# Performance work log

Hardware: AMD Instinct MI355X
Metric: run time of the kernel (lower is better)

The kernel has to match this reference:

```python
import jax, jax.numpy as jnp
import numpy as np

B, T, C, H = 4, 4096, 1024, 64

def setup_inputs() -> dict:
    key = jax.random.key(0)
    k1, k2, k3, k4 = jax.random.split(key, 4)
    x = jax.random.normal(k1, (B, T, C), dtype=jnp.float32)
    # nn.Linear(C, H, bias=False): y = x @ W^T with W [H, C]; store as [C, H] for x @ W
    Wq = jax.random.normal(k2, (C, H), dtype=jnp.float32) * (C ** -0.5)
    Wk = jax.random.normal(k3, (C, H), dtype=jnp.float32) * (C ** -0.5)
    Wv = jax.random.normal(k4, (C, H), dtype=jnp.float32) * (C ** -0.5)
    return {"x": x, "Wq": Wq, "Wk": Wk, "Wv": Wv}

def reference(x, Wq, Wk, Wv):
    # Manual causal single-head attention (dropout p=0 -> identity).
    q = x @ Wq  # [B, T, H]
    k = x @ Wk  # [B, T, H]
    v = x @ Wv  # [B, T, H]
    scale = q.shape[-1] ** -0.5
    w = jnp.einsum('bth,bsh->bts', q, k) * scale  # [B, T, T] scores
    causal = jnp.tril(jnp.ones((x.shape[1], x.shape[1]), dtype=bool))
    w = jnp.where(causal, w, -jnp.inf)
    w = jax.nn.softmax(w, axis=-1)
    out = jnp.einsum('bts,bsh->bth', w, v)  # [B, T, H]
    return out
```

## Files before the change

### kernel.cpp

```cpp
#include <hip/hip_runtime.h>
#include <math.h>

#define Bn 4
#define Tn 4096
#define Cn 1024
#define Hn 64

typedef __attribute__((ext_vector_type(8))) short short8;
typedef __attribute__((ext_vector_type(4))) float floatx4;
typedef unsigned short ushort_t;

#define QSCALE 0.1803368801111204f

#define ILP_FENCE() asm volatile("" ::: "memory")

__device__ __forceinline__ ushort_t f2bf(float f) {
  union { float f; unsigned u; } v; v.f = f;
  unsigned r = v.u + 0x7FFFu + ((v.u >> 16) & 1u);
  return (ushort_t)(r >> 16);
}
__device__ __forceinline__ ushort_t f2bf_hu(float f) {
  union { float f; unsigned u; } v; v.f = f;
  return (ushort_t)((v.u + 0x8000u) >> 16);
}
__device__ __forceinline__ float bf2f(ushort_t h) {
  union { unsigned u; float f; } v; v.u = ((unsigned)h) << 16; return v.f;
}


__global__ __launch_bounds__(256) void wf_kernel(
    const float* __restrict__ Wq, const float* __restrict__ Wk,
    const float* __restrict__ Wv, ushort_t* __restrict__ Wf)
{
  __shared__ float ws[32][65];
  const int tid = threadIdx.x;
  const int m = blockIdx.x >> 5;
  const int g = blockIdx.x & 31;
  const float* W = (m == 0) ? Wq : (m == 1) ? Wk : Wv;
  const float4* src = (const float4*)(W + (size_t)g * 32 * Hn);
#pragma unroll
  for (int it = 0; it < 2; ++it) {
    int i4 = it * 256 + tid;
    float4 v = src[i4];
    int c = i4 >> 4, h = (i4 & 15) * 4;
    ws[c][h] = v.x; ws[c][h + 1] = v.y; ws[c][h + 2] = v.z; ws[c][h + 3] = v.w;
  }
  __syncthreads();
  const int nt = tid >> 6, lane = tid & 63;
  const int col = lane & 15, quad = lane >> 4;
  ushort_t t[8];
#pragma unroll
  for (int e = 0; e < 8; ++e) t[e] = f2bf(ws[quad * 8 + e][nt * 16 + col]);
  *(short8*)(Wf + ((size_t)((m * 32 + g) * 4 + nt) * 64 + lane) * 8) = *(short8*)t;
}

__global__ __launch_bounds__(256, 2) void qkv_proj_kernel(
    const float* __restrict__ x, const ushort_t* __restrict__ Wf,
    ushort_t* __restrict__ Qf, ushort_t* __restrict__ Kf,
    ushort_t* __restrict__ Vf)
{
  __shared__ __align__(16) char smem[67584];
  ushort_t* xs  = (ushort_t*)smem;
  ushort_t* red = (ushort_t*)smem;
  ushort_t* img = (ushort_t*)(smem + 49152);

  const int tid  = threadIdx.x;
  const int wv   = tid >> 6;
  const int lane = tid & 63;
  const int col  = lane & 15;
  const int quad = lane >> 4;
  const int blk  = blockIdx.x;
  const int row0 = blk * 32;

#pragma unroll
  for (int half = 0; half < 2; ++half) {
    float4 v[16];
#pragma unroll
    for (int jj = 0; jj < 16; ++jj)
      v[jj] = *(const float4*)(x + (size_t)(row0 + half * 16 + jj) * Cn + wv * 256 + lane * 4);
    ILP_FENCE();
#pragma unroll
    for (int jj = 0; jj < 16; ++jj) {
      ushort4 u;
      u.x = f2bf(v[jj].x); u.y = f2bf(v[jj].y); u.z = f2bf(v[jj].z); u.w = f2bf(v[jj].w);
      *(ushort4*)(xs + (wv * 32 + half * 16 + jj) * 264 + lane * 4) = u;
    }
  }

  floatx4 acc[2][3][4];
#pragma unroll
  for (int sub = 0; sub < 2; ++sub)
#pragma unroll
    for (int m = 0; m < 3; ++m)
#pragma unroll
      for (int nt = 0; nt < 4; ++nt) {
        acc[sub][m][nt][0] = 0.f; acc[sub][m][nt][1] = 0.f;
        acc[sub][m][nt][2] = 0.f; acc[sub][m][nt][3] = 0.f;
      }

#pragma unroll
  for (int ch = 0; ch < 8; ++ch) {
    const int gg = wv * 8 + ch;
    short8 bf[12];
#pragma unroll
    for (int k = 0; k < 12; ++k) {
      const int m_ = k >> 2, nt_ = k & 3;
      bf[k] = *(const short8*)(Wf + ((size_t)((m_ * 32 + gg) * 4 + nt_) * 64 + lane) * 8);
    }
    short8 af0 = *(const short8*)(xs + (wv * 32 + col) * 264 + ch * 32 + quad * 8);
    short8 af1 = *(const short8*)(xs + (wv * 32 + 16 + col) * 264 + ch * 32 + quad * 8);
    ILP_FENCE();
#pragma unroll
    for (int k = 0; k < 12; ++k) {
      const int m_ = k >> 2, nt_ = k & 3;
      acc[0][m_][nt_] = __builtin_amdgcn_mfma_f32_16x16x32_bf16(af0, bf[k], acc[0][m_][nt_], 0, 0, 0);
      acc[1][m_][nt_] = __builtin_amdgcn_mfma_f32_16x16x32_bf16(af1, bf[k], acc[1][m_][nt_], 0, 0, 0);
    }
  }
  __syncthreads();

#pragma unroll
  for (int sub = 0; sub < 2; ++sub)
#pragma unroll
    for (int m = 0; m < 3; ++m)
#pragma unroll
      for (int nt = 0; nt < 4; ++nt) {
        const int p = (sub * 3 + m) * 4 + nt;
        ushort4 u;
        u.x = f2bf(acc[sub][m][nt][0]); u.y = f2bf(acc[sub][m][nt][1]);
        u.z = f2bf(acc[sub][m][nt][2]); u.w = f2bf(acc[sub][m][nt][3]);
        *(ushort4*)&red[((p * 4 + wv) * 64 + lane) * 4] = u;
      }
  __syncthreads();

#pragma unroll
  for (int pp = 0; pp < 6; ++pp) {
    const int p = wv * 6 + pp;
    ushort4 w0 = *(const ushort4*)&red[((p * 4 + 0) * 64 + lane) * 4];
    ushort4 w1 = *(const ushort4*)&red[((p * 4 + 1) * 64 + lane) * 4];
    ushort4 w2 = *(const ushort4*)&red[((p * 4 + 2) * 64 + lane) * 4];
    ushort4 w3 = *(const ushort4*)&red[((p * 4 + 3) * 64 + lane) * 4];
    float v[4];
    v[0] = (bf2f(w0.x) + bf2f(w1.x)) + (bf2f(w2.x) + bf2f(w3.x));
    v[1] = (bf2f(w0.y) + bf2f(w1.y)) + (bf2f(w2.y) + bf2f(w3.y));
    v[2] = (bf2f(w0.z) + bf2f(w1.z)) + (bf2f(w2.z) + bf2f(w3.z));
    v[3] = (bf2f(w0.w) + bf2f(w1.w)) + (bf2f(w2.w) + bf2f(w3.w));
    const int sub = (p >= 12) ? 1 : 0;
    const int mrem = p - sub * 12;
    const int m = mrem >> 2, nt = mrem & 3;
#pragma unroll
    for (int r = 0; r < 4; ++r) {
      const int tlq = quad * 4 + r;
      if (m == 2) {
        img[4096 + nt * 512 + (quad * 16 + col) * 8 + sub * 4 + r] = f2bf(v[r]);
      } else {
        const int h = nt * 16 + col;
        const int idx = (h >> 5) * 512 + ((h >> 3) & 3) * 128 + tlq * 8 + (h & 7);
        img[m * 2048 + sub * 1024 + idx] = f2bf(m == 0 ? v[r] * QSCALE : v[r]);
      }
    }
  }
  __syncthreads();

  {
    const int b = blk >> 7, g = blk & 127;
#pragma unroll
    for (int sub = 0; sub < 2; ++sub) {
      const size_t qg = (size_t)(b * 256 + 2 * g + sub) * 1024 + tid * 4;
      *(uint2*)(Qf + qg) = *(const uint2*)&img[sub * 1024 + tid * 4];
      *(uint2*)(Kf + qg) = *(const uint2*)&img[2048 + sub * 1024 + tid * 4];
    }
    const int ht = tid >> 6;
    const size_t vg = ((size_t)(b * 64 + (g >> 1)) * 8 + ht * 2 + (g & 1)) * 512 + (tid & 63) * 8;
    *(short8*)(Vf + vg) = *(const short8*)&img[4096 + ht * 512 + (tid & 63) * 8];
  }
}

__global__ __launch_bounds__(256, 2) void attn_kernel(
    const ushort_t* __restrict__ Qf, const ushort_t* __restrict__ Kf,
    const ushort_t* __restrict__ Vf, float* __restrict__ out)
{
  __shared__ __align__(16) float Om[4][2][16][68];
  __shared__ __align__(16) float Ml[4][2][16];

  const int tid  = threadIdx.x;
  const int wv   = tid >> 6;
  const int lane = tid & 63;
  const int col  = lane & 15;
  const int quad = lane >> 4;
  const int b   = blockIdx.x & 3;
  const int idx = blockIdx.x >> 2;
  const int g   = (idx < 64) ? (127 - 2 * idx) : (2 * (idx - 64));

  short8 qf[2][2];
#pragma unroll
  for (int sub = 0; sub < 2; ++sub)
#pragma unroll
    for (int half = 0; half < 2; ++half)
      qf[sub][half] = *(const short8*)(Qf + (size_t)(b * 256 + 2 * g + sub) * 1024 + half * 512 + lane * 8);

  const ushort_t* Kbase = Kf + (size_t)b * 256 * 1024;
  const ushort_t* Vbase = Vf + (size_t)b * 64 * 8 * 512;

  short8 ones;
#pragma unroll
  for (int e = 0; e < 8; ++e) ones[e] = (short)0x3F80;

  floatx4 o[2][4], ol[2];
#pragma unroll
  for (int sub = 0; sub < 2; ++sub) {
#pragma unroll
    for (int ht = 0; ht < 4; ++ht) { o[sub][ht][0]=0.f; o[sub][ht][1]=0.f; o[sub][ht][2]=0.f; o[sub][ht][3]=0.f; }
    ol[sub][0]=0.f; ol[sub][1]=0.f; ol[sub][2]=0.f; ol[sub][3]=0.f;
  }

  const int ntile = ((g * 32 + 31) >> 6) + 1;
  const int dtile = ntile - 1;

  for (int i = wv; i < ntile; i += 4) {
    short8 kf[8], vf[8];
#pragma unroll
    for (int kt = 0; kt < 4; ++kt) {
      const ushort_t* kp = Kbase + (size_t)i * 4096 + kt * 1024 + lane * 8;
      kf[kt * 2]     = *(const short8*)(kp);
      kf[kt * 2 + 1] = *(const short8*)(kp + 512);
    }
#pragma unroll
    for (int ht = 0; ht < 4; ++ht) {
#pragma unroll
      for (int kh = 0; kh < 2; ++kh)
        vf[ht * 2 + kh] = *(const short8*)(Vbase + ((size_t)i * 8 + ht * 2 + kh) * 512 + lane * 8);
    }
    ILP_FENCE();

    floatx4 s[2][4];
    __builtin_amdgcn_s_setprio(1);
#pragma unroll
    for (int sub = 0; sub < 2; ++sub)
#pragma unroll
      for (int kt = 0; kt < 4; ++kt) {
        floatx4 c; c[0]=0.f; c[1]=0.f; c[2]=0.f; c[3]=0.f;
        c = __builtin_amdgcn_mfma_f32_16x16x32_bf16(kf[kt * 2],     qf[sub][0], c, 0, 0, 0);
        c = __builtin_amdgcn_mfma_f32_16x16x32_bf16(kf[kt * 2 + 1], qf[sub][1], c, 0, 0, 0);
        s[sub][kt] = c;
      }
    __builtin_amdgcn_s_setprio(0);

    if (i == dtile) {
#pragma unroll
      for (int sub = 0; sub < 2; ++sub)
#pragma unroll
        for (int kt = 0; kt < 4; ++kt)
#pragma unroll
          for (int r = 0; r < 4; ++r)
            if (64 * i + kt * 16 + quad * 4 + r > g * 32 + sub * 16 + col)
              s[sub][kt][r] = -INFINITY;
    }

#pragma unroll
    for (int sub = 0; sub < 2; ++sub)
#pragma unroll
      for (int kt = 0; kt < 4; ++kt)
#pragma unroll
        for (int r = 0; r < 4; ++r)
          s[sub][kt][r] = __builtin_amdgcn_exp2f(s[sub][kt][r]);

    short8 pf[2][2];
#pragma unroll
    for (int sub = 0; sub < 2; ++sub)
#pragma unroll
      for (int kh = 0; kh < 2; ++kh) {
        ushort_t tmp[8];
#pragma unroll
        for (int half = 0; half < 2; ++half)
#pragma unroll
          for (int r = 0; r < 4; ++r)
            tmp[half * 4 + r] = f2bf_hu(s[sub][2 * kh + half][r]);
        pf[sub][kh] = *(short8*)tmp;
      }

    __builtin_amdgcn_s_setprio(1);
#pragma unroll
    for (int sub = 0; sub < 2; ++sub) {
#pragma unroll
      for (int ht = 0; ht < 4; ++ht) {
        o[sub][ht] = __builtin_amdgcn_mfma_f32_16x16x32_bf16(pf[sub][0], vf[ht * 2],     o[sub][ht], 0, 0, 0);
        o[sub][ht] = __builtin_amdgcn_mfma_f32_16x16x32_bf16(pf[sub][1], vf[ht * 2 + 1], o[sub][ht], 0, 0, 0);
      }
      ol[sub] = __builtin_amdgcn_mfma_f32_16x16x32_bf16(pf[sub][0], ones, ol[sub], 0, 0, 0);
      ol[sub] = __builtin_amdgcn_mfma_f32_16x16x32_bf16(pf[sub][1], ones, ol[sub], 0, 0, 0);
    }
    __builtin_amdgcn_s_setprio(0);
  }

#pragma unroll
  for (int sub = 0; sub < 2; ++sub) {
#pragma unroll
    for (int ht = 0; ht < 4; ++ht)
#pragma unroll
      for (int r = 0; r < 4; ++r)
        Om[wv][sub][quad * 4 + r][ht * 16 + col] = o[sub][ht][r];
    if (col == 0) {
#pragma unroll
      for (int r = 0; r < 4; ++r) Ml[wv][sub][quad * 4 + r] = ol[sub][r];
    }
  }
  __syncthreads();

  const int rr = tid >> 4, h4 = (tid & 15) * 4;
#pragma unroll
  for (int sub = 0; sub < 2; ++sub) {
    float L = (Ml[0][sub][rr] + Ml[1][sub][rr]) + (Ml[2][sub][rr] + Ml[3][sub][rr]);
    float4 a; a.x = 0.f; a.y = 0.f; a.z = 0.f; a.w = 0.f;
#pragma unroll
    for (int w = 0; w < 4; ++w) {
      float4 ov = *(const float4*)&Om[w][sub][rr][h4];
      a.x += ov.x; a.y += ov.y; a.z += ov.z; a.w += ov.w;
    }
    float inv = 1.f / L;
    a.x *= inv; a.y *= inv; a.z *= inv; a.w *= inv;
    *(float4*)(out + (size_t)(b * Tn + g * 32 + sub * 16 + rr) * Hn + h4) = a;
  }
}

extern "C" void kernel_launch(void* const* d_in, const int* in_sizes, int n_in,
                              void* d_out, int out_size, void* d_ws, size_t ws_size,
                              hipStream_t stream) {
  const float* x  = (const float*)d_in[0];
  const float* Wq = (const float*)d_in[1];
  const float* Wk = (const float*)d_in[2];
  const float* Wv = (const float*)d_in[3];
  float* out = (float*)d_out;

  ushort_t* Qf = (ushort_t*)d_ws;
  ushort_t* Kf = Qf + (size_t)Bn * Tn * Hn;
  ushort_t* Vf = Kf + (size_t)Bn * Tn * Hn;
  ushort_t* Wf = Vf + (size_t)Bn * Tn * Hn;

  wf_kernel<<<dim3(96), dim3(256), 0, stream>>>(Wq, Wk, Wv, Wf);
  qkv_proj_kernel<<<dim3(512), dim3(256), 0, stream>>>(x, Wf, Qf, Kf, Vf);
  attn_kernel<<<dim3(Bn * 128), dim3(256), 0, stream>>>(Qf, Kf, Vf, out);
}
```

Baseline: 123.3 us.

## Load x via direct global-to-LDS DMA and halve projection block rows

The QKV projection kernel now stages fp32 x rows straight into shared memory with global_load_lds, using an XOR swizzle, instead of loading into registers, converting to bf16 and storing. Conversion to bf16 moves to the A-fragment read inside the MFMA loop. Each block now handles 16 rows rather than 32, so twice as many blocks are launched and each keeps half as many accumulators, with the Q/K/V write-out indexing updated to match. The aim is to reduce register pressure and staging overhead and to raise parallelism, at the cost of reloading the weight fragments from global memory in twice as many blocks.

```diff
diff --git a/kernel.cpp b/kernel.cpp
--- a/kernel.cpp
+++ b/kernel.cpp
@@ -13,6 +13,12 @@
 #define QSCALE 0.1803368801111204f
 
 #define ILP_FENCE() asm volatile("" ::: "memory")
+
+__device__ __forceinline__ void dma16(const void* g, void* l) {
+  __builtin_amdgcn_global_load_lds(
+      (const __attribute__((address_space(1))) void*)g,
+      (__attribute__((address_space(3))) void*)l, 16, 0, 0);
+}
 
 __device__ __forceinline__ ushort_t f2bf(float f) {
   union { float f; unsigned u; } v; v.f = f;
@@ -59,10 +65,9 @@
     ushort_t* __restrict__ Qf, ushort_t* __restrict__ Kf,
     ushort_t* __restrict__ Vf)
 {
-  __shared__ __align__(16) char smem[67584];
-  ushort_t* xs  = (ushort_t*)smem;
+  __shared__ __align__(16) char smem[65536];
   ushort_t* red = (ushort_t*)smem;
-  ushort_t* img = (ushort_t*)(smem + 49152);
+  ushort_t* img = (ushort_t*)(smem + 24576);
 
   const int tid  = threadIdx.x;
   const int wv   = tid >> 6;
@@ -70,33 +75,25 @@
   const int col  = lane & 15;
   const int quad = lane >> 4;
   const int blk  = blockIdx.x;
-  const int row0 = blk * 32;
-
-#pragma unroll
-  for (int half = 0; half < 2; ++half) {
-    float4 v[16];
-#pragma unroll
-    for (int jj = 0; jj < 16; ++jj)
-      v[jj] = *(const float4*)(x + (size_t)(row0 + half * 16 + jj) * Cn + wv * 256 + lane * 4);
-    ILP_FENCE();
-#pragma unroll
-    for (int jj = 0; jj < 16; ++jj) {
-      ushort4 u;
-      u.x = f2bf(v[jj].x); u.y = f2bf(v[jj].y); u.z = f2bf(v[jj].z); u.w = f2bf(v[jj].w);
-      *(ushort4*)(xs + (wv * 32 + half * 16 + jj) * 264 + lane * 4) = u;
-    }
-  }
-
-  floatx4 acc[2][3][4];
-#pragma unroll
-  for (int sub = 0; sub < 2; ++sub)
-#pragma unroll
-    for (int m = 0; m < 3; ++m)
-#pragma unroll
-      for (int nt = 0; nt < 4; ++nt) {
-        acc[sub][m][nt][0] = 0.f; acc[sub][m][nt][1] = 0.f;
-        acc[sub][m][nt][2] = 0.f; acc[sub][m][nt][3] = 0.f;
-      }
+  const int row0 = blk * 16;
+
+#pragma unroll
+  for (int r = 0; r < 16; ++r) {
+    const float* gp = x + (size_t)(row0 + r) * Cn + wv * 256 + ((lane ^ (r & 7)) << 2);
+    void* lp = smem + wv * 16384 + r * 1024;
+    dma16(gp, lp);
+  }
+  asm volatile("s_waitcnt vmcnt(0)" ::: "memory");
+  __builtin_amdgcn_sched_barrier(0);
+
+  floatx4 acc[3][4];
+#pragma unroll
+  for (int m = 0; m < 3; ++m)
+#pragma unroll
+    for (int nt = 0; nt < 4; ++nt) {
+      acc[m][nt][0] = 0.f; acc[m][nt][1] = 0.f;
+      acc[m][nt][2] = 0.f; acc[m][nt][3] = 0.f;
+    }
 
 #pragma unroll
   for (int ch = 0; ch < 8; ++ch) {
@@ -107,35 +104,35 @@
       const int m_ = k >> 2, nt_ = k & 3;
       bf[k] = *(const short8*)(Wf + ((size_t)((m_ * 32 + gg) * 4 + nt_) * 64 + lane) * 8);
     }
-    short8 af0 = *(const short8*)(xs + (wv * 32 + col) * 264 + ch * 32 + quad * 8);
-    short8 af1 = *(const short8*)(xs + (wv * 32 + 16 + col) * 264 + ch * 32 + quad * 8);
+    const int c0 = ch * 8 + quad * 2;
+    float4 va = *(const float4*)(smem + wv * 16384 + col * 1024 + ((c0 ^ (col & 7)) << 4));
+    float4 vb = *(const float4*)(smem + wv * 16384 + col * 1024 + (((c0 + 1) ^ (col & 7)) << 4));
     ILP_FENCE();
-#pragma unroll
-    for (int k = 0; k < 12; ++k) {
-      const int m_ = k >> 2, nt_ = k & 3;
-      acc[0][m_][nt_] = __builtin_amdgcn_mfma_f32_16x16x32_bf16(af0, bf[k], acc[0][m_][nt_], 0, 0, 0);
-      acc[1][m_][nt_] = __builtin_amdgcn_mfma_f32_16x16x32_bf16(af1, bf[k], acc[1][m_][nt_], 0, 0, 0);
-    }
-  }
-  __syncthreads();
-
-#pragma unroll
-  for (int sub = 0; sub < 2; ++sub)
-#pragma unroll
-    for (int m = 0; m < 3; ++m)
-#pragma unroll
-      for (int nt = 0; nt < 4; ++nt) {
-        const int p = (sub * 3 + m) * 4 + nt;
-        ushort4 u;
-        u.x = f2bf(acc[sub][m][nt][0]); u.y = f2bf(acc[sub][m][nt][1]);
-        u.z = f2bf(acc[sub][m][nt][2]); u.w = f2bf(acc[sub][m][nt][3]);
-        *(ushort4*)&red[((p * 4 + wv) * 64 + lane) * 4] = u;
-      }
-  __syncthreads();
-
-#pragma unroll
-  for (int pp = 0; pp < 6; ++pp) {
-    const int p = wv * 6 + pp;
+    ushort_t t[8];
+    t[0] = f2bf(va.x); t[1] = f2bf(va.y); t[2] = f2bf(va.z); t[3] = f2bf(va.w);
+    t[4] = f2bf(vb.x); t[5] = f2bf(vb.y); t[6] = f2bf(vb.z); t[7] = f2bf(vb.w);
+    short8 af = *(short8*)t;
+#pragma unroll
+    for (int k = 0; k < 12; ++k)
+      acc[k >> 2][k & 3] = __builtin_amdgcn_mfma_f32_16x16x32_bf16(af, bf[k], acc[k >> 2][k & 3], 0, 0, 0);
+  }
+  __syncthreads();
+
+#pragma unroll
+  for (int m = 0; m < 3; ++m)
+#pragma unroll
+    for (int nt = 0; nt < 4; ++nt) {
+      const int p = m * 4 + nt;
+      ushort4 u;
+      u.x = f2bf(acc[m][nt][0]); u.y = f2bf(acc[m][nt][1]);
+      u.z = f2bf(acc[m][nt][2]); u.w = f2bf(acc[m][nt][3]);
+      *(ushort4*)&red[((p * 4 + wv) * 64 + lane) * 4] = u;
+    }
+  __syncthreads();
+
+#pragma unroll
+  for (int pp = 0; pp < 3; ++pp) {
+    const int p = wv * 3 + pp;
     ushort4 w0 = *(const ushort4*)&red[((p * 4 + 0) * 64 + lane) * 4];
     ushort4 w1 = *(const ushort4*)&red[((p * 4 + 1) * 64 + lane) * 4];
     ushort4 w2 = *(const ushort4*)&red[((p * 4 + 2) * 64 + lane) * 4];
@@ -145,34 +142,30 @@
     v[1] = (bf2f(w0.y) + bf2f(w1.y)) + (bf2f(w2.y) + bf2f(w3.y));
     v[2] = (bf2f(w0.z) + bf2f(w1.z)) + (bf2f(w2.z) + bf2f(w3.z));
     v[3] = (bf2f(w0.w) + bf2f(w1.w)) + (bf2f(w2.w) + bf2f(w3.w));
-    const int sub = (p >= 12) ? 1 : 0;
-    const int mrem = p - sub * 12;
-    const int m = mrem >> 2, nt = mrem & 3;
+    const int m = p >> 2, nt = p & 3;
 #pragma unroll
     for (int r = 0; r < 4; ++r) {
       const int tlq = quad * 4 + r;
       if (m == 2) {
-        img[4096 + nt * 512 + (quad * 16 + col) * 8 + sub * 4 + r] = f2bf(v[r]);
+        img[2048 + nt * 256 + (quad * 16 + col) * 4 + r] = f2bf(v[r]);
       } else {
         const int h = nt * 16 + col;
         const int idx = (h >> 5) * 512 + ((h >> 3) & 3) * 128 + tlq * 8 + (h & 7);
-        img[m * 2048 + sub * 1024 + idx] = f2bf(m == 0 ? v[r] * QSCALE : v[r]);
+        img[m * 1024 + idx] = f2bf(m == 0 ? v[r] * QSCALE : v[r]);
       }
     }
   }
   __syncthreads();
 
   {
-    const int b = blk >> 7, g = blk & 127;
-#pragma unroll
-    for (int sub = 0; sub < 2; ++sub) {
-      const size_t qg = (size_t)(b * 256 + 2 * g + sub) * 1024 + tid * 4;
-      *(uint2*)(Qf + qg) = *(const uint2*)&img[sub * 1024 + tid * 4];
-      *(uint2*)(Kf + qg) = *(const uint2*)&img[2048 + sub * 1024 + tid * 4];
-    }
+    const int b = blk >> 8, g = blk & 255;
+    const size_t qg = (size_t)(b * 256 + g) * 1024 + tid * 4;
+    *(uint2*)(Qf + qg) = *(const uint2*)&img[tid * 4];
+    *(uint2*)(Kf + qg) = *(const uint2*)&img[1024 + tid * 4];
     const int ht = tid >> 6;
-    const size_t vg = ((size_t)(b * 64 + (g >> 1)) * 8 + ht * 2 + (g & 1)) * 512 + (tid & 63) * 8;
-    *(short8*)(Vf + vg) = *(const short8*)&img[4096 + ht * 512 + (tid & 63) * 8];
+    const size_t vg = ((size_t)(b * 64 + (g >> 2)) * 8 + ht * 2 + ((g >> 1) & 1)) * 512
+                      + (tid & 63) * 8 + (g & 1) * 4;
+    *(uint2*)(Vf + vg) = *(const uint2*)&img[2048 + ht * 256 + (tid & 63) * 4];
   }
 }
 
@@ -338,6 +331,6 @@
   ushort_t* Wf = Vf + (size_t)Bn * Tn * Hn;
 
   wf_kernel<<<dim3(96), dim3(256), 0, stream>>>(Wq, Wk, Wv, Wf);
-  qkv_proj_kernel<<<dim3(512), dim3(256), 0, stream>>>(x, Wf, Qf, Kf, Vf);
+  qkv_proj_kernel<<<dim3(1024), dim3(256), 0, stream>>>(x, Wf, Qf, Kf, Vf);
   attn_kernel<<<dim3(Bn * 128), dim3(256), 0, stream>>>(Qf, Kf, Vf, out);
 }
```

Measured after the change: 126.8 us. 1.03x slower.

## Process 64 rows per block in QKV projection to reuse weight fragments

Applied to the files above, without the earlier changes.

The QKV projection block now handles 64 tokens instead of 32, so each weight fragment loaded from global memory feeds four MFMA row tiles instead of two. This halves the grid to 256 blocks and doubles shared memory to about 132 KB, with launch bounds lowered to one block per CU. The aim is to cut redundant weight traffic per token. The cost is fewer blocks (256 on a 256-CU part), lower occupancy and more accumulator registers, which may reduce latency hiding.

```diff
diff --git a/kernel.cpp b/kernel.cpp
--- a/kernel.cpp
+++ b/kernel.cpp
@@ -54,15 +54,15 @@
   *(short8*)(Wf + ((size_t)((m * 32 + g) * 4 + nt) * 64 + lane) * 8) = *(short8*)t;
 }
 
-__global__ __launch_bounds__(256, 2) void qkv_proj_kernel(
+__global__ __launch_bounds__(256, 1) void qkv_proj_kernel(
     const float* __restrict__ x, const ushort_t* __restrict__ Wf,
     ushort_t* __restrict__ Qf, ushort_t* __restrict__ Kf,
     ushort_t* __restrict__ Vf)
 {
-  __shared__ __align__(16) char smem[67584];
+  __shared__ __align__(16) char smem[135168];
   ushort_t* xs  = (ushort_t*)smem;
   ushort_t* red = (ushort_t*)smem;
-  ushort_t* img = (ushort_t*)(smem + 49152);
+  ushort_t* img = (ushort_t*)(smem + 98304);
 
   const int tid  = threadIdx.x;
   const int wv   = tid >> 6;
@@ -70,33 +70,31 @@
   const int col  = lane & 15;
   const int quad = lane >> 4;
   const int blk  = blockIdx.x;
-  const int row0 = blk * 32;
-
-#pragma unroll
-  for (int half = 0; half < 2; ++half) {
+  const int row0 = blk * 64;
+
+#pragma unroll
+  for (int b4 = 0; b4 < 4; ++b4) {
     float4 v[16];
 #pragma unroll
     for (int jj = 0; jj < 16; ++jj)
-      v[jj] = *(const float4*)(x + (size_t)(row0 + half * 16 + jj) * Cn + wv * 256 + lane * 4);
+      v[jj] = *(const float4*)(x + (size_t)(row0 + b4 * 16 + jj) * Cn + wv * 256 + lane * 4);
     ILP_FENCE();
 #pragma unroll
     for (int jj = 0; jj < 16; ++jj) {
       ushort4 u;
       u.x = f2bf(v[jj].x); u.y = f2bf(v[jj].y); u.z = f2bf(v[jj].z); u.w = f2bf(v[jj].w);
-      *(ushort4*)(xs + (wv * 32 + half * 16 + jj) * 264 + lane * 4) = u;
-    }
-  }
-
-  floatx4 acc[2][3][4];
-#pragma unroll
-  for (int sub = 0; sub < 2; ++sub)
-#pragma unroll
-    for (int m = 0; m < 3; ++m)
-#pragma unroll
-      for (int nt = 0; nt < 4; ++nt) {
-        acc[sub][m][nt][0] = 0.f; acc[sub][m][nt][1] = 0.f;
-        acc[sub][m][nt][2] = 0.f; acc[sub][m][nt][3] = 0.f;
-      }
+      *(ushort4*)(xs + (wv * 64 + b4 * 16 + jj) * 264 + lane * 4) = u;
+    }
+  }
+
+  floatx4 acc[4][12];
+#pragma unroll
+  for (int sub = 0; sub < 4; ++sub)
+#pragma unroll
+    for (int k = 0; k < 12; ++k) {
+      acc[sub][k][0] = 0.f; acc[sub][k][1] = 0.f;
+      acc[sub][k][2] = 0.f; acc[sub][k][3] = 0.f;
+    }
 
 #pragma unroll
   for (int ch = 0; ch < 8; ++ch) {
@@ -107,35 +105,34 @@
       const int m_ = k >> 2, nt_ = k & 3;
       bf[k] = *(const short8*)(Wf + ((size_t)((m_ * 32 + gg) * 4 + nt_) * 64 + lane) * 8);
     }
-    short8 af0 = *(const short8*)(xs + (wv * 32 + col) * 264 + ch * 32 + quad * 8);
-    short8 af1 = *(const short8*)(xs + (wv * 32 + 16 + col) * 264 + ch * 32 + quad * 8);
+    short8 af[4];
+#pragma unroll
+    for (int sub = 0; sub < 4; ++sub)
+      af[sub] = *(const short8*)(xs + (wv * 64 + sub * 16 + col) * 264 + ch * 32 + quad * 8);
     ILP_FENCE();
 #pragma unroll
+    for (int k = 0; k < 12; ++k)
+#pragma unroll
+      for (int sub = 0; sub < 4; ++sub)
+        acc[sub][k] = __builtin_amdgcn_mfma_f32_16x16x32_bf16(af[sub], bf[k], acc[sub][k], 0, 0, 0);
+  }
+  __syncthreads();
+
+#pragma unroll
+  for (int sub = 0; sub < 4; ++sub)
+#pragma unroll
     for (int k = 0; k < 12; ++k) {
-      const int m_ = k >> 2, nt_ = k & 3;
-      acc[0][m_][nt_] = __builtin_amdgcn_mfma_f32_16x16x32_bf16(af0, bf[k], acc[0][m_][nt_], 0, 0, 0);
-      acc[1][m_][nt_] = __builtin_amdgcn_mfma_f32_16x16x32_bf16(af1, bf[k], acc[1][m_][nt_], 0, 0, 0);
-    }
-  }
-  __syncthreads();
-
-#pragma unroll
-  for (int sub = 0; sub < 2; ++sub)
-#pragma unroll
-    for (int m = 0; m < 3; ++m)
-#pragma unroll
-      for (int nt = 0; nt < 4; ++nt) {
-        const int p = (sub * 3 + m) * 4 + nt;
-        ushort4 u;
-        u.x = f2bf(acc[sub][m][nt][0]); u.y = f2bf(acc[sub][m][nt][1]);
-        u.z = f2bf(acc[sub][m][nt][2]); u.w = f2bf(acc[sub][m][nt][3]);
-        *(ushort4*)&red[((p * 4 + wv) * 64 + lane) * 4] = u;
-      }
-  __syncthreads();
-
-#pragma unroll
-  for (int pp = 0; pp < 6; ++pp) {
-    const int p = wv * 6 + pp;
+      const int p = sub * 12 + k;
+      ushort4 u;
+      u.x = f2bf(acc[sub][k][0]); u.y = f2bf(acc[sub][k][1]);
+      u.z = f2bf(acc[sub][k][2]); u.w = f2bf(acc[sub][k][3]);
+      *(ushort4*)&red[((p * 4 + wv) * 64 + lane) * 4] = u;
+    }
+  __syncthreads();
+
+#pragma unroll
+  for (int pp = 0; pp < 12; ++pp) {
+    const int p = wv * 12 + pp;
     ushort4 w0 = *(const ushort4*)&red[((p * 4 + 0) * 64 + lane) * 4];
     ushort4 w1 = *(const ushort4*)&red[((p * 4 + 1) * 64 + lane) * 4];
     ushort4 w2 = *(const ushort4*)&red[((p * 4 + 2) * 64 + lane) * 4];
@@ -145,34 +142,32 @@
     v[1] = (bf2f(w0.y) + bf2f(w1.y)) + (bf2f(w2.y) + bf2f(w3.y));
     v[2] = (bf2f(w0.z) + bf2f(w1.z)) + (bf2f(w2.z) + bf2f(w3.z));
     v[3] = (bf2f(w0.w) + bf2f(w1.w)) + (bf2f(w2.w) + bf2f(w3.w));
-    const int sub = (p >= 12) ? 1 : 0;
-    const int mrem = p - sub * 12;
-    const int m = mrem >> 2, nt = mrem & 3;
+    const int m = pp >> 2, nt = pp & 3;
 #pragma unroll
     for (int r = 0; r < 4; ++r) {
       const int tlq = quad * 4 + r;
       if (m == 2) {
-        img[4096 + nt * 512 + (quad * 16 + col) * 8 + sub * 4 + r] = f2bf(v[r]);
+        img[8192 + nt * 1024 + (wv >> 1) * 512 + (quad * 16 + col) * 8 + (wv & 1) * 4 + r] = f2bf(v[r]);
       } else {
         const int h = nt * 16 + col;
         const int idx = (h >> 5) * 512 + ((h >> 3) & 3) * 128 + tlq * 8 + (h & 7);
-        img[m * 2048 + sub * 1024 + idx] = f2bf(m == 0 ? v[r] * QSCALE : v[r]);
+        img[m * 4096 + wv * 1024 + idx] = f2bf(m == 0 ? v[r] * QSCALE : v[r]);
       }
     }
   }
   __syncthreads();
 
   {
-    const int b = blk >> 7, g = blk & 127;
-#pragma unroll
-    for (int sub = 0; sub < 2; ++sub) {
-      const size_t qg = (size_t)(b * 256 + 2 * g + sub) * 1024 + tid * 4;
+    const int b = blk >> 6, gp = blk & 63;
+#pragma unroll
+    for (int sub = 0; sub < 4; ++sub) {
+      const size_t qg = (size_t)(b * 256 + gp * 4 + sub) * 1024 + tid * 4;
       *(uint2*)(Qf + qg) = *(const uint2*)&img[sub * 1024 + tid * 4];
-      *(uint2*)(Kf + qg) = *(const uint2*)&img[2048 + sub * 1024 + tid * 4];
-    }
-    const int ht = tid >> 6;
-    const size_t vg = ((size_t)(b * 64 + (g >> 1)) * 8 + ht * 2 + (g & 1)) * 512 + (tid & 63) * 8;
-    *(short8*)(Vf + vg) = *(const short8*)&img[4096 + ht * 512 + (tid & 63) * 8];
+      *(uint2*)(Kf + qg) = *(const uint2*)&img[4096 + sub * 1024 + tid * 4];
+    }
+    const size_t vbase = ((size_t)(b * 64 + gp) * 8) * 512;
+    *(short8*)(Vf + vbase + tid * 8)        = *(const short8*)&img[8192 + tid * 8];
+    *(short8*)(Vf + vbase + 2048 + tid * 8) = *(const short8*)&img[8192 + 2048 + tid * 8];
   }
 }
 
@@ -338,6 +333,6 @@
   ushort_t* Wf = Vf + (size_t)Bn * Tn * Hn;
 
   wf_kernel<<<dim3(96), dim3(256), 0, stream>>>(Wq, Wk, Wv, Wf);
-  qkv_proj_kernel<<<dim3(512), dim3(256), 0, stream>>>(x, Wf, Qf, Kf, Vf);
+  qkv_proj_kernel<<<dim3(256), dim3(256), 0, stream>>>(x, Wf, Qf, Kf, Vf);
   attn_kernel<<<dim3(Bn * 128), dim3(256), 0, stream>>>(Qf, Kf, Vf, out);
 }
```

Result: no change. 125.7 us (+2.0%).
